# Performance work log

Hardware: AMD Instinct MI355X
Metric: run time of the kernel (lower is better)

## Reference

```python
import jax, jax.numpy as jnp
import numpy as np

D_MODEL = 1024
N_HEADS = 16
D_HEAD = 64
BATCH = 4
SEQ = 2048
NEG = -1000000000.0


def setup_inputs() -> dict:
    key = jax.random.key(0)
    k1, k2, k3, k4, k5 = jax.random.split(key, 5)
    x = jax.random.normal(k1, (BATCH, SEQ, D_MODEL), dtype=jnp.float32)
    std = 0.02
    wq = jax.random.normal(k2, (N_HEADS, D_HEAD, D_MODEL), dtype=jnp.float32) * std
    wk = jax.random.normal(k3, (N_HEADS, D_HEAD, D_MODEL), dtype=jnp.float32) * std
    wv = jax.random.normal(k4, (N_HEADS, D_HEAD, D_MODEL), dtype=jnp.float32) * std
    wo = jax.random.normal(k5, (D_MODEL, N_HEADS * D_HEAD), dtype=jnp.float32) * std
    return {"x": x, "wq": wq, "wk": wk, "wv": wv, "wo": wo}


def reference(x, wq, wk, wv, wo):
    # x: [b, s, d_model]; wq/wk/wv: [h, d_head, d_model]; wo: [d_model, h*d_head]
    b, s, _ = x.shape
    scale = jnp.sqrt(jnp.asarray(D_HEAD, x.dtype))
    q = jnp.einsum('bsd,hed->bhse', x, wq)
    k = jnp.einsum('bsd,hed->bhse', x, wk)
    v = jnp.einsum('bsd,hed->bhse', x, wv)
    scores = jnp.einsum('bhse,bhte->bhst', q, k) / scale
    causal_mask = jnp.triu(jnp.ones((s, s), dtype=bool), k=1)
    scores = jnp.where(causal_mask, jnp.asarray(NEG, scores.dtype), scores)
    weights = jax.nn.softmax(scores, axis=-1)
    heads = jnp.einsum('bhst,bhte->bhse', weights, v)  # [b, h, s, d_head]
    concat = heads.transpose(0, 2, 1, 3).reshape(b, s, N_HEADS * D_HEAD)
    return concat @ wo.T
```

## Files before the change

kernel.cpp:

```cpp
#include <hip/hip_runtime.h>


#define DEV __device__ __forceinline__

typedef __attribute__((ext_vector_type(8))) __bf16 bf16x8;
typedef __attribute__((ext_vector_type(4))) float f32x4;
typedef unsigned short u16;

struct alignas(8) U16x4 { u16 x, y, z, w; };

DEV u16 f2bf(float f) {
  unsigned int u = __builtin_bit_cast(unsigned int, f);
  u = u + 0x7FFFu + ((u >> 16) & 1u);
  return (u16)(u >> 16);
}

DEV unsigned cvt_pk_bf16(float a, float b) {
  unsigned r;
  asm("v_cvt_pk_bf16_f32 %0, %1, %2" : "=v"(r) : "v"(a), "v"(b));
  return r;
}

DEV void gload_lds16(const void* g, void* l) {
  __builtin_amdgcn_global_load_lds(
      (const __attribute__((address_space(1))) unsigned int*)g,
      (__attribute__((address_space(3))) unsigned int*)l, 16, 0, 0);
}

__global__ void cast_kernel(const float* __restrict__ in, u16* __restrict__ out, int n4) {
  int i = blockIdx.x * blockDim.x + threadIdx.x;
  if (i >= n4) return;
  const float4 v = reinterpret_cast<const float4*>(in)[i];
  U16x4 o{f2bf(v.x), f2bf(v.y), f2bf(v.z), f2bf(v.w)};
  reinterpret_cast<U16x4*>(out)[i] = o;
}

__global__ void cast_w_kernel(const float* __restrict__ wq, const float* __restrict__ wk,
                              const float* __restrict__ wv, const float* __restrict__ wo,
                              u16* __restrict__ wqkvb, u16* __restrict__ wob) {
  const int y = blockIdx.y;
  const int i = blockIdx.x * blockDim.x + threadIdx.x;
  const float* src = (y == 0) ? wq : (y == 1) ? wk : (y == 2) ? wv : wo;
  u16* dst = (y < 3) ? (wqkvb + (size_t)y * 1048576) : wob;
  const float4 v = reinterpret_cast<const float4*>(src)[i];
  U16x4 o{f2bf(v.x), f2bf(v.y), f2bf(v.z), f2bf(v.w)};
  reinterpret_cast<U16x4*>(dst)[i] = o;
}

template <int MODE, int NBN>
__global__ __launch_bounds__(256) void gemm_bt(
    const u16* __restrict__ A, const u16* __restrict__ B,
    void* __restrict__ C0, u16* __restrict__ vtp, int N) {
  constexpr int K = 1024;
  const int d = blockIdx.x;
  const int chunk = gridDim.x >> 3;
  const int vg = (d & 7) * chunk + (d >> 3);
  const int bn = vg % NBN, bm = vg / NBN;
  const int tid = threadIdx.x;
  const int w = tid >> 6, lane = tid & 63, lo = lane & 15, hi = lane >> 4;
  const int wm = w >> 1, wn = w & 1;

  __shared__ char lds[65536];
  char* sA = lds;
  char* sB = lds + 32768;

  const u16* Ag = A + (size_t)(bm * 128) * K;
  const u16* Bg = B + (size_t)(bn * 128) * K;

  f32x4 acc[4][4] = {};

  auto stage = [&](int buf, int k0) {
#pragma unroll
    for (int it = 0; it < 4; ++it) {
      const int L = (it * 4 + w) * 64 + lane;
      const int r = L >> 3, p = L & 7, c = p ^ (r & 7);
      gload_lds16(Ag + (size_t)r * K + k0 + c * 8, sA + buf * 16384 + (it * 4 + w) * 1024);
      gload_lds16(Bg + (size_t)r * K + k0 + c * 8, sB + buf * 16384 + (it * 4 + w) * 1024);
    }
  };

  stage(0, 0);
  __syncthreads();
  int cur = 0;
  for (int t = 0; t < 16; ++t) {
    if (t + 1 < 16) stage(cur ^ 1, (t + 1) * 64);
#pragma unroll
    for (int kc = 0; kc < 2; ++kc) {
      bf16x8 af[4], bfr[4];
#pragma unroll
      for (int m = 0; m < 4; ++m) {
        const int r = wm * 64 + m * 16 + lo;
        const int p = (kc * 4 + hi) ^ (r & 7);
        af[m] = *reinterpret_cast<const bf16x8*>(sA + cur * 16384 + r * 128 + p * 16);
      }
#pragma unroll
      for (int n = 0; n < 4; ++n) {
        const int r = wn * 64 + n * 16 + lo;
        const int p = (kc * 4 + hi) ^ (r & 7);
        bfr[n] = *reinterpret_cast<const bf16x8*>(sB + cur * 16384 + r * 128 + p * 16);
      }
#pragma unroll
      for (int m = 0; m < 4; ++m)
#pragma unroll
        for (int n = 0; n < 4; ++n)
          acc[m][n] = __builtin_amdgcn_mfma_f32_16x16x32_bf16(af[m], bfr[n], acc[m][n], 0, 0, 0);
    }
    __syncthreads();
    cur ^= 1;
  }

  const int colW = bn * 128 + wn * 64;
  const int rowW = bm * 128 + wm * 64;
  if (MODE == 0) {
    float* C = (float*)C0;
#pragma unroll
    for (int m = 0; m < 4; ++m)
#pragma unroll
      for (int n = 0; n < 4; ++n) {
        const int col = colW + n * 16 + lo;
        const int rb = rowW + m * 16 + hi * 4;
#pragma unroll
        for (int rg = 0; rg < 4; ++rg)
          C[(size_t)(rb + rg) * N + col] = acc[m][n][rg];
      }
  } else {
    u16* qkvp = (u16*)C0;
    if (bn * 128 < 2048) {
      const float qs = (bn < 8) ? 0.18033688011112042f : 1.0f;
#pragma unroll
      for (int m = 0; m < 4; ++m)
#pragma unroll
        for (int n = 0; n < 4; ++n) {
          const int col = colW + n * 16 + lo;
          const int rb = rowW + m * 16 + hi * 4;
#pragma unroll
          for (int rg = 0; rg < 4; ++rg)
            qkvp[(size_t)(rb + rg) * 2048 + col] = f2bf(acc[m][n][rg] * qs);
        }
    } else {
#pragma unroll
      for (int m = 0; m < 4; ++m)
#pragma unroll
        for (int n = 0; n < 4; ++n) {
          const int col = colW + n * 16 + lo;
          const int idx = col - 2048;
          const int hh = idx >> 6, e = idx & 63;
          const int rb = rowW + m * 16 + hi * 4;
          const int bb = rb >> 11, s = rb & 2047;
          U16x4 v4{f2bf(acc[m][n][0]), f2bf(acc[m][n][1]),
                   f2bf(acc[m][n][2]), f2bf(acc[m][n][3])};
          *reinterpret_cast<U16x4*>(vtp + ((size_t)((bb * 16 + hh) * 64 + e)) * 2048 + s) = v4;
        }
    }
  }
}

__global__ __launch_bounds__(512, 4) void attn_kernel(
    const u16* __restrict__ qkv, const u16* __restrict__ vt, u16* __restrict__ heads) {
  const int dd = blockIdx.x;
  const int vg = (dd & 7) * 64 + (dd >> 3);
  const int bx = vg & 7, bh = vg >> 3;
  const int b = bh >> 4, h = bh & 15;
  const int tid = threadIdx.x;
  const int w = tid >> 6, lane = tid & 63, lo = lane & 15, hi = lane >> 4;

  __shared__ char lds[49152];
  char* sQP = lds;
  char* sK  = lds + 16384;
  char* sV  = lds + 32768;

  const u16* Kg = qkv + (size_t)(b * 2048) * 2048 + 1024 + h * 64;
  const u16* Vg = vt + (size_t)bh * 64 * 2048;

  const int sr = tid >> 3, sc = (tid & 7) ^ (sr & 7);
  auto stageKV = [&](int buf, int kv0) {
    gload_lds16(Kg + (size_t)(kv0 + sr) * 2048 + sc * 8, sK + buf * 8192 + w * 1024);
    gload_lds16(Vg + (size_t)sr * 2048 + kv0 + sc * 8, sV + buf * 8192 + w * 1024);
  };

  char* sP = sQP + w * 2048;

  for (int rep = 0; rep < 2; ++rep) {
    const int qt = rep ? (15 - bx) : bx;
    const u16* Qg = qkv + (size_t)(b * 2048 + qt * 128) * 2048 + h * 64;

#pragma unroll
    for (int it = 0; it < 2; ++it) {
      const int r = it * 64 + sr;
      gload_lds16(Qg + (size_t)r * 2048 + sc * 8, sQP + it * 8192 + w * 1024);
    }
    stageKV(0, 0);
    __syncthreads();

    bf16x8 qf[2];
#pragma unroll
    for (int kc = 0; kc < 2; ++kc) {
      const int r = w * 16 + lo;
      const int p = (kc * 4 + hi) ^ (r & 7);
      qf[kc] = *reinterpret_cast<const bf16x8*>(sQP + r * 128 + p * 16);
    }
    __syncthreads();

    float mreg = -1e30f, lrow = 0.f;
    f32x4 oacc[4] = {};

    const int nt = 2 * (qt + 1);
    const int qrow = qt * 128 + w * 16 + lo;
    const int qmax = qt * 128 + w * 16 + 15;

    auto step = [&](int t, int cur) {
      if (t + 1 < nt) stageKV(cur ^ 1, (t + 1) * 64);
      if (t * 64 <= qmax) {
        f32x4 sa[4] = {};
        __builtin_amdgcn_s_setprio(1);
#pragma unroll
        for (int kc = 0; kc < 2; ++kc) {
#pragma unroll
          for (int n = 0; n < 4; ++n) {
            const int r = n * 16 + lo;
            const int p = (kc * 4 + hi) ^ (lo & 7);
            const bf16x8 kf = *reinterpret_cast<const bf16x8*>(sK + cur * 8192 + r * 128 + p * 16);
            sa[n] = __builtin_amdgcn_mfma_f32_16x16x32_bf16(kf, qf[kc], sa[n], 0, 0, 0);
          }
        }
        __builtin_amdgcn_s_setprio(0);

        if (t >= nt - 2) {
#pragma unroll
          for (int n = 0; n < 4; ++n)
#pragma unroll
            for (int rg = 0; rg < 4; ++rg)
              if (t * 64 + n * 16 + hi * 4 + rg > qrow) sa[n][rg] = -1e9f;
        }

        const f32x4 vm2 = __builtin_elementwise_max(__builtin_elementwise_max(sa[0], sa[1]),
                                                    __builtin_elementwise_max(sa[2], sa[3]));
        float pm = fmaxf(fmaxf(vm2[0], vm2[1]), fmaxf(vm2[2], vm2[3]));
        pm = fmaxf(pm, __shfl_xor(pm, 16));
        pm = fmaxf(pm, __shfl_xor(pm, 32));
        if (!__all(pm <= mreg + 8.0f)) {
          const float mn = fmaxf(mreg, pm);
          const float alpha = exp2f(mreg - mn);
          mreg = mn;
          lrow *= alpha;
#pragma unroll
          for (int ne = 0; ne < 4; ++ne) oacc[ne] *= alpha;
        }
        f32x4 pe[4];
#pragma unroll
        for (int n = 0; n < 4; ++n) {
          const f32x4 dv = sa[n] - mreg;
#pragma unroll
          for (int rg = 0; rg < 4; ++rg) pe[n][rg] = exp2f(dv[rg]);
        }
        const f32x4 vs = (pe[0] + pe[1]) + (pe[2] + pe[3]);
        lrow += (vs[0] + vs[1]) + (vs[2] + vs[3]);

#pragma unroll
        for (int n = 0; n < 4; ++n) {
          const unsigned w0 = cvt_pk_bf16(pe[n][0], pe[n][1]);
          const unsigned w1 = cvt_pk_bf16(pe[n][2], pe[n][3]);
          const int Hp = 2 * (n & 1) + (hi >> 1);
          *reinterpret_cast<uint2*>(sP + (n >> 1) * 1024 + Hp * 256 +
                                    ((lo ^ Hp) << 4) + ((hi & 1) << 3)) = uint2{w0, w1};
        }
        bf16x8 pf[2];
#pragma unroll
        for (int kc = 0; kc < 2; ++kc)
          pf[kc] = *reinterpret_cast<const bf16x8*>(sP + kc * 1024 + hi * 256 + ((lo ^ hi) << 4));

        __builtin_amdgcn_s_setprio(1);
#pragma unroll
        for (int kc = 0; kc < 2; ++kc) {
#pragma unroll
          for (int ne = 0; ne < 4; ++ne) {
            const int r = ne * 16 + lo;
            const int p = (kc * 4 + hi) ^ (lo & 7);
            const bf16x8 vf = *reinterpret_cast<const bf16x8*>(sV + cur * 8192 + r * 128 + p * 16);
            oacc[ne] = __builtin_amdgcn_mfma_f32_16x16x32_bf16(vf, pf[kc], oacc[ne], 0, 0, 0);
          }
        }
        __builtin_amdgcn_s_setprio(0);
      }
      __syncthreads();
    };

    for (int i = 0; i < nt; i += 2) {
      step(i, 0);
      step(i + 1, 1);
    }

    float lsum = lrow;
    lsum += __shfl_xor(lsum, 16);
    lsum += __shfl_xor(lsum, 32);
    const float inv = 1.0f / lsum;
    const int q = qt * 128 + w * 16 + lo;
    u16* dst = heads + (size_t)(b * 2048 + q) * 1024 + h * 64;
#pragma unroll
    for (int ne = 0; ne < 4; ++ne) {
      const unsigned r0 = cvt_pk_bf16(oacc[ne][0] * inv, oacc[ne][1] * inv);
      const unsigned r1 = cvt_pk_bf16(oacc[ne][2] * inv, oacc[ne][3] * inv);
      *reinterpret_cast<uint2*>(dst + ne * 16 + hi * 4) = uint2{r0, r1};
    }
  }
}

extern "C" void kernel_launch(void* const* d_in, const int* in_sizes, int n_in,
                              void* d_out, int out_size, void* d_ws, size_t ws_size,
                              hipStream_t stream) {
  const float* x  = (const float*)d_in[0];
  const float* wq = (const float*)d_in[1];
  const float* wk = (const float*)d_in[2];
  const float* wv = (const float*)d_in[3];
  const float* wo = (const float*)d_in[4];

  char* ws = (char*)d_ws;
  u16* xb    = (u16*)(ws);
  u16* wqkvb = (u16*)(ws + 16777216);
  u16* wob   = (u16*)(ws + 23068672);
  u16* qkv   = (u16*)(ws + 25165824);
  u16* vtp   = (u16*)(ws + 58720256);
  u16* heads = (u16*)(ws + 75497472);

  cast_kernel<<<8192, 256, 0, stream>>>(x, xb, 2097152);
  cast_w_kernel<<<dim3(1024, 4), 256, 0, stream>>>(wq, wk, wv, wo, wqkvb, wob);

  gemm_bt<1, 24><<<1536, 256, 0, stream>>>(xb, wqkvb, qkv, vtp, 3072);
  attn_kernel<<<512, 512, 0, stream>>>(qkv, vtp, heads);
  gemm_bt<0, 8><<<512, 256, 0, stream>>>(heads, wob, d_out, nullptr, 1024);
}
```

Before: 186.5 us.

## Process 128-key tiles per step in causal flash attention kernel

Doubles the KV tile from 64 to 128 keys per iteration, halving the number of steps and block-wide barriers per query tile. LDS grows to 80KB with larger double-buffered K and V staging, and V rows now hold 128 keys. This drops the per-warp skip of fully masked subtiles, so on the diagonal tile some warps now compute fully masked work. The larger LDS footprint may also cut how many blocks fit on a CU.

```diff
diff --git a/kernel.cpp b/kernel.cpp
--- a/kernel.cpp
+++ b/kernel.cpp
@@ -164,120 +164,126 @@
   const int tid = threadIdx.x;
   const int w = tid >> 6, lane = tid & 63, lo = lane & 15, hi = lane >> 4;
 
-  __shared__ char lds[49152];
+  __shared__ char lds[81920];
   char* sQP = lds;
   char* sK  = lds + 16384;
-  char* sV  = lds + 32768;
+  char* sV  = lds + 49152;
 
   const u16* Kg = qkv + (size_t)(b * 2048) * 2048 + 1024 + h * 64;
   const u16* Vg = vt + (size_t)bh * 64 * 2048;
 
-  const int sr = tid >> 3, sc = (tid & 7) ^ (sr & 7);
+  const int kr = tid >> 3, kc_ = (tid & 7) ^ (kr & 7);
+  const int vr = tid >> 4, vc_ = (tid & 15) ^ (vr & 7);
   auto stageKV = [&](int buf, int kv0) {
-    gload_lds16(Kg + (size_t)(kv0 + sr) * 2048 + sc * 8, sK + buf * 8192 + w * 1024);
-    gload_lds16(Vg + (size_t)sr * 2048 + kv0 + sc * 8, sV + buf * 8192 + w * 1024);
+#pragma unroll
+    for (int it = 0; it < 2; ++it) {
+      gload_lds16(Kg + (size_t)(kv0 + it * 64 + kr) * 2048 + kc_ * 8,
+                  sK + buf * 16384 + it * 8192 + w * 1024);
+      gload_lds16(Vg + (size_t)(it * 32 + vr) * 2048 + kv0 + vc_ * 8,
+                  sV + buf * 16384 + it * 8192 + w * 1024);
+    }
   };
 
   char* sP = sQP + w * 2048;
+  const int qloc = w * 16 + lo;
 
   for (int rep = 0; rep < 2; ++rep) {
     const int qt = rep ? (15 - bx) : bx;
     const u16* Qg = qkv + (size_t)(b * 2048 + qt * 128) * 2048 + h * 64;
 
 #pragma unroll
-    for (int it = 0; it < 2; ++it) {
-      const int r = it * 64 + sr;
-      gload_lds16(Qg + (size_t)r * 2048 + sc * 8, sQP + it * 8192 + w * 1024);
-    }
+    for (int it = 0; it < 2; ++it)
+      gload_lds16(Qg + (size_t)(it * 64 + kr) * 2048 + kc_ * 8, sQP + it * 8192 + w * 1024);
     stageKV(0, 0);
     __syncthreads();
 
     bf16x8 qf[2];
 #pragma unroll
     for (int kc = 0; kc < 2; ++kc) {
-      const int r = w * 16 + lo;
-      const int p = (kc * 4 + hi) ^ (r & 7);
-      qf[kc] = *reinterpret_cast<const bf16x8*>(sQP + r * 128 + p * 16);
+      const int p = (kc * 4 + hi) ^ (lo & 7);
+      qf[kc] = *reinterpret_cast<const bf16x8*>(sQP + qloc * 128 + p * 16);
     }
     __syncthreads();
 
     float mreg = -1e30f, lrow = 0.f;
     f32x4 oacc[4] = {};
 
-    const int nt = 2 * (qt + 1);
-    const int qrow = qt * 128 + w * 16 + lo;
-    const int qmax = qt * 128 + w * 16 + 15;
+    const int nt = qt + 1;
 
     auto step = [&](int t, int cur) {
-      if (t + 1 < nt) stageKV(cur ^ 1, (t + 1) * 64);
-      if (t * 64 <= qmax) {
-        f32x4 sa[4] = {};
+      if (t + 1 < nt) stageKV(cur ^ 1, (t + 1) * 128);
+      f32x4 sa[8] = {};
+      __builtin_amdgcn_s_setprio(1);
+#pragma unroll
+      for (int kc = 0; kc < 2; ++kc) {
+#pragma unroll
+        for (int n = 0; n < 8; ++n) {
+          const int r = n * 16 + lo;
+          const int p = (kc * 4 + hi) ^ (lo & 7);
+          const bf16x8 kf = *reinterpret_cast<const bf16x8*>(sK + cur * 16384 + r * 128 + p * 16);
+          sa[n] = __builtin_amdgcn_mfma_f32_16x16x32_bf16(kf, qf[kc], sa[n], 0, 0, 0);
+        }
+      }
+      __builtin_amdgcn_s_setprio(0);
+
+      if (t == nt - 1) {
+#pragma unroll
+        for (int n = 0; n < 8; ++n)
+#pragma unroll
+          for (int rg = 0; rg < 4; ++rg)
+            if (n * 16 + hi * 4 + rg > qloc) sa[n][rg] = -1e9f;
+      }
+
+      f32x4 vm = __builtin_elementwise_max(sa[0], sa[1]);
+#pragma unroll
+      for (int n = 2; n < 8; ++n) vm = __builtin_elementwise_max(vm, sa[n]);
+      float pm = fmaxf(fmaxf(vm[0], vm[1]), fmaxf(vm[2], vm[3]));
+      pm = fmaxf(pm, __shfl_xor(pm, 16));
+      pm = fmaxf(pm, __shfl_xor(pm, 32));
+      if (!__all(pm <= mreg + 8.0f)) {
+        const float mn = fmaxf(mreg, pm);
+        const float alpha = exp2f(mreg - mn);
+        mreg = mn;
+        lrow *= alpha;
+#pragma unroll
+        for (int ne = 0; ne < 4; ++ne) oacc[ne] *= alpha;
+      }
+#pragma unroll
+      for (int n = 0; n < 8; ++n) {
+        const f32x4 dv = sa[n] - mreg;
+#pragma unroll
+        for (int rg = 0; rg < 4; ++rg) sa[n][rg] = exp2f(dv[rg]);
+      }
+      f32x4 vs = sa[0] + sa[1];
+#pragma unroll
+      for (int n = 2; n < 8; ++n) vs += sa[n];
+      lrow += (vs[0] + vs[1]) + (vs[2] + vs[3]);
+
+#pragma unroll
+      for (int kh = 0; kh < 2; ++kh) {
+#pragma unroll
+        for (int n4 = 0; n4 < 4; ++n4) {
+          const int n = kh * 4 + n4;
+          const unsigned w0 = cvt_pk_bf16(sa[n][0], sa[n][1]);
+          const unsigned w1 = cvt_pk_bf16(sa[n][2], sa[n][3]);
+          const int Hp = 2 * (n4 & 1) + (hi >> 1);
+          *reinterpret_cast<uint2*>(sP + (n4 >> 1) * 1024 + Hp * 256 +
+                                    ((lo ^ Hp) << 4) + ((hi & 1) << 3)) = uint2{w0, w1};
+        }
+        bf16x8 pf[2];
+#pragma unroll
+        for (int kcl = 0; kcl < 2; ++kcl)
+          pf[kcl] = *reinterpret_cast<const bf16x8*>(sP + kcl * 1024 + hi * 256 + ((lo ^ hi) << 4));
+
         __builtin_amdgcn_s_setprio(1);
 #pragma unroll
-        for (int kc = 0; kc < 2; ++kc) {
-#pragma unroll
-          for (int n = 0; n < 4; ++n) {
-            const int r = n * 16 + lo;
-            const int p = (kc * 4 + hi) ^ (lo & 7);
-            const bf16x8 kf = *reinterpret_cast<const bf16x8*>(sK + cur * 8192 + r * 128 + p * 16);
-            sa[n] = __builtin_amdgcn_mfma_f32_16x16x32_bf16(kf, qf[kc], sa[n], 0, 0, 0);
-          }
-        }
-        __builtin_amdgcn_s_setprio(0);
-
-        if (t >= nt - 2) {
-#pragma unroll
-          for (int n = 0; n < 4; ++n)
-#pragma unroll
-            for (int rg = 0; rg < 4; ++rg)
-              if (t * 64 + n * 16 + hi * 4 + rg > qrow) sa[n][rg] = -1e9f;
-        }
-
-        const f32x4 vm2 = __builtin_elementwise_max(__builtin_elementwise_max(sa[0], sa[1]),
-                                                    __builtin_elementwise_max(sa[2], sa[3]));
-        float pm = fmaxf(fmaxf(vm2[0], vm2[1]), fmaxf(vm2[2], vm2[3]));
-        pm = fmaxf(pm, __shfl_xor(pm, 16));
-        pm = fmaxf(pm, __shfl_xor(pm, 32));
-        if (!__all(pm <= mreg + 8.0f)) {
-          const float mn = fmaxf(mreg, pm);
-          const float alpha = exp2f(mreg - mn);
-          mreg = mn;
-          lrow *= alpha;
-#pragma unroll
-          for (int ne = 0; ne < 4; ++ne) oacc[ne] *= alpha;
-        }
-        f32x4 pe[4];
-#pragma unroll
-        for (int n = 0; n < 4; ++n) {
-          const f32x4 dv = sa[n] - mreg;
-#pragma unroll
-          for (int rg = 0; rg < 4; ++rg) pe[n][rg] = exp2f(dv[rg]);
-        }
-        const f32x4 vs = (pe[0] + pe[1]) + (pe[2] + pe[3]);
-        lrow += (vs[0] + vs[1]) + (vs[2] + vs[3]);
-
-#pragma unroll
-        for (int n = 0; n < 4; ++n) {
-          const unsigned w0 = cvt_pk_bf16(pe[n][0], pe[n][1]);
-          const unsigned w1 = cvt_pk_bf16(pe[n][2], pe[n][3]);
-          const int Hp = 2 * (n & 1) + (hi >> 1);
-          *reinterpret_cast<uint2*>(sP + (n >> 1) * 1024 + Hp * 256 +
-                                    ((lo ^ Hp) << 4) + ((hi & 1) << 3)) = uint2{w0, w1};
-        }
-        bf16x8 pf[2];
-#pragma unroll
-        for (int kc = 0; kc < 2; ++kc)
-          pf[kc] = *reinterpret_cast<const bf16x8*>(sP + kc * 1024 + hi * 256 + ((lo ^ hi) << 4));
-
-        __builtin_amdgcn_s_setprio(1);
-#pragma unroll
-        for (int kc = 0; kc < 2; ++kc) {
+        for (int kcl = 0; kcl < 2; ++kcl) {
 #pragma unroll
           for (int ne = 0; ne < 4; ++ne) {
             const int r = ne * 16 + lo;
-            const int p = (kc * 4 + hi) ^ (lo & 7);
-            const bf16x8 vf = *reinterpret_cast<const bf16x8*>(sV + cur * 8192 + r * 128 + p * 16);
-            oacc[ne] = __builtin_amdgcn_mfma_f32_16x16x32_bf16(vf, pf[kc], oacc[ne], 0, 0, 0);
+            const int s = ((2 * kh + kcl) * 4 + hi) ^ (lo & 7);
+            const bf16x8 vf = *reinterpret_cast<const bf16x8*>(sV + cur * 16384 + r * 256 + s * 16);
+            oacc[ne] = __builtin_amdgcn_mfma_f32_16x16x32_bf16(vf, pf[kcl], oacc[ne], 0, 0, 0);
           }
         }
         __builtin_amdgcn_s_setprio(0);
@@ -287,14 +293,14 @@
 
     for (int i = 0; i < nt; i += 2) {
       step(i, 0);
-      step(i + 1, 1);
+      if (i + 1 < nt) step(i + 1, 1);
     }
 
     float lsum = lrow;
     lsum += __shfl_xor(lsum, 16);
     lsum += __shfl_xor(lsum, 32);
     const float inv = 1.0f / lsum;
-    const int q = qt * 128 + w * 16 + lo;
+    const int q = qt * 128 + qloc;
     u16* dst = heads + (size_t)(b * 2048 + q) * 1024 + h * 64;
 #pragma unroll
     for (int ne = 0; ne < 4; ++ne) {
```

Result: no change. 184.6 us (-1.0%).
